# Optimization experiments

Hardware: AMD Instinct MI355X
Metric: run time of the kernel (lower is better)

## Reference

```python
import jax, jax.numpy as jnp
import numpy as np


def setup_inputs() -> dict:
    key = jax.random.key(0)
    k1, k2, k3, k4, k5, k6 = jax.random.split(key, 6)
    Ne, dim_in, dim_out, B, Nr, E = 100000, 128, 128, 4, 8, 200000
    return {
        "H": jax.random.normal(k1, (Ne, dim_in), dtype=jnp.float32),
        "A": jax.random.uniform(k2, (Nr, B), dtype=jnp.float32),
        "V": jax.random.uniform(k3, (B, dim_in, dim_out), dtype=jnp.float32),
        "edge_row": jax.random.randint(k4, (Nr, E), 0, Ne, dtype=jnp.int32),
        "edge_col": jax.random.randint(k5, (Nr, E), 0, Ne, dtype=jnp.int32),
        "edge_val": jax.random.uniform(k6, (Nr, E), dtype=jnp.float32),
    }


def reference(H, A, V, edge_row, edge_col, edge_val):
    # W = einsum('rb,bio->rio', A, V): basis-decomposed relation weights
    Ne = H.shape[0]
    Nr = A.shape[0]
    W = jnp.einsum('rb,bio->rio', A, V)            # [Nr, dim_in, dim_out]
    HxW = jnp.einsum('ni,rio->rno', H, W)          # [Nr, Ne, dim_out]
    # sparse T_r @ HxW_r: gather source rows (cols of T), scale by values,
    # scatter-add into destination rows. Done for all relations at once.
    msgs = HxW[jnp.arange(Nr)[:, None], edge_col] * edge_val[..., None]  # [Nr, E, dim_out]
    out = jax.ops.segment_sum(
        msgs.reshape(-1, msgs.shape[-1]),
        edge_row.reshape(-1),
        num_segments=Ne,
    )  # sum over relations folded into one segment_sum
    return out
```

## Files before the change

### kernel.cpp

```cpp
#include <hip/hip_runtime.h>

typedef __attribute__((ext_vector_type(8))) short short8;
typedef __attribute__((ext_vector_type(4))) float floatx4;

constexpr int DIM   = 128;
constexpr int NB    = 4;
constexpr int NR    = 8;
constexpr int BROWS = 512;
constexpr int BCAP  = 16384;

static __device__ __forceinline__ unsigned short f2bf(float f) {
    unsigned int u = __float_as_uint(f);
    u += 0x7FFFu + ((u >> 16) & 1u);
    return (unsigned short)(u >> 16);
}
static __device__ __forceinline__ float bf_lo(unsigned int h) {
    return __uint_as_float(h << 16);
}
static __device__ __forceinline__ float bf_hi(unsigned int h) {
    return __uint_as_float(h & 0xFFFF0000u);
}

__global__ __launch_bounds__(256) void build_vfrag(
    const float* __restrict__ V, unsigned short* __restrict__ VfragG)
{
    int idx  = blockIdx.x * 256 + threadIdx.x;
    int lane = idx & 63;
    int ks   = (idx >> 6) & 3;
    int ot   = (idx >> 8) & 7;
    int b    = idx >> 11;

    int o  = ot * 16 + (lane & 15);
    int kb = ks * 32 + (lane >> 4) * 8;

    short8 v;
#pragma unroll
    for (int j = 0; j < 8; ++j)
        v[j] = (short)f2bf(V[((size_t)b * DIM + kb + j) * DIM + o]);
    *reinterpret_cast<short8*>(VfragG + (size_t)idx * 8) = v;
}

__global__ __launch_bounds__(256) void build_wfrag(
    const float* __restrict__ A, const float* __restrict__ V,
    unsigned short* __restrict__ Wfrag)
{
    int idx  = blockIdx.x * 256 + threadIdx.x;
    int lane = idx & 63;
    int ks   = (idx >> 6) & 3;
    int ot   = (idx >> 8) & 7;
    int r    = idx >> 11;

    int o     = ot * 16 + (lane & 15);
    int kbase = ks * 32 + (lane >> 4) * 8;

    float a0 = A[r * NB + 0], a1 = A[r * NB + 1];
    float a2 = A[r * NB + 2], a3 = A[r * NB + 3];

    short8 v;
#pragma unroll
    for (int j = 0; j < 8; ++j) {
        int k = kbase + j;
        float w = a0 * V[(0 * DIM + k) * DIM + o]
                + a1 * V[(1 * DIM + k) * DIM + o]
                + a2 * V[(2 * DIM + k) * DIM + o]
                + a3 * V[(3 * DIM + k) * DIM + o];
        v[j] = (short)f2bf(w);
    }
    *reinterpret_cast<short8*>(Wfrag + (size_t)idx * 8) = v;
}

__global__ __launch_bounds__(256) void h_to_bf(
    const float* __restrict__ H, unsigned short* __restrict__ Hbf, int n8)
{
    int i = blockIdx.x * 256 + threadIdx.x;
    if (i >= n8) return;
    const float4* hp = reinterpret_cast<const float4*>(H) + (size_t)i * 2;
    float4 f0 = hp[0];
    float4 f1 = hp[1];
    short8 v;
    v[0] = (short)f2bf(f0.x); v[1] = (short)f2bf(f0.y);
    v[2] = (short)f2bf(f0.z); v[3] = (short)f2bf(f0.w);
    v[4] = (short)f2bf(f1.x); v[5] = (short)f2bf(f1.y);
    v[6] = (short)f2bf(f1.z); v[7] = (short)f2bf(f1.w);
    *reinterpret_cast<short8*>(Hbf + (size_t)i * 8) = v;
}

__global__ __launch_bounds__(256) void bucket_scatter(
    const int* __restrict__ erow, const int* __restrict__ ecol,
    const float* __restrict__ eval, int* __restrict__ bcnt,
    int2* __restrict__ sorted1, int n, int E, int chunk)
{
    __shared__ int cnt[256];
    __shared__ int base[256];
    int t = threadIdx.x;
    cnt[t] = 0;
    __syncthreads();

    int s = blockIdx.x * chunk;
    int e = s + chunk; if (e > n) e = n;

    for (int i = s + t; i < e; i += 256)
        atomicAdd(&cnt[erow[i] >> 9], 1);
    __syncthreads();

    int c = cnt[t];
    base[t] = (c > 0) ? atomicAdd(&bcnt[t], c) : 0;
    cnt[t] = 0;
    __syncthreads();

    for (int i = s + t; i < e; i += 256) {
        int row = erow[i];
        int bkt = row >> 9;
        int rank = atomicAdd(&cnt[bkt], 1);
        int r = (int)((unsigned)i / (unsigned)E);
        int2 m;
        m.x = ((row & (BROWS - 1)) << 20) | (r << 17) | ecol[i];
        m.y = __float_as_int(eval[i]);
        sorted1[(size_t)bkt * BCAP + base[bkt] + rank] = m;
    }
}

__global__ __launch_bounds__(256) void bucket_scan(
    const int* __restrict__ bcnt, int* __restrict__ bstart,
    int* __restrict__ rowStart, int nbuc, int Ne)
{
    __shared__ int sd[256];
    int t = threadIdx.x;
    int c = (t < nbuc) ? bcnt[t] : 0;
    sd[t] = c; __syncthreads();
#pragma unroll
    for (int off = 1; off < 256; off <<= 1) {
        int v = (t >= off) ? sd[t - off] : 0;
        __syncthreads();
        sd[t] += v;
        __syncthreads();
    }
    if (t < nbuc) bstart[t] = sd[t] - c;
    if (t == nbuc - 1) rowStart[Ne] = sd[t];
}

__global__ __launch_bounds__(256) void bucket_sort(
    const int2* __restrict__ sorted1, const int* __restrict__ bcnt,
    const int* __restrict__ bstart, int* __restrict__ rowStart,
    int2* __restrict__ sorted, int Ne)
{
    __shared__ int hcnt[BROWS];
    __shared__ int hoff[BROWS];
    int b = blockIdx.x;
    int t = threadIdx.x;
    hcnt[t] = 0; hcnt[t + 256] = 0;
    __syncthreads();

    int n = bcnt[b];
    const int2* src = sorted1 + (size_t)b * BCAP;

    for (int i = t; i < n; i += 256)
        atomicAdd(&hcnt[(unsigned)src[i].x >> 20], 1);
    __syncthreads();

    if (t == 0) {
        int run = 0;
#pragma unroll 8
        for (int j = 0; j < BROWS; ++j) { hoff[j] = run; run += hcnt[j]; }
    }
    __syncthreads();

    int bs = bstart[b];
    int rs = b * BROWS;
    int nr = Ne - rs; if (nr > BROWS) nr = BROWS;
    for (int j = t; j < nr; j += 256)
        rowStart[rs + j] = bs + hoff[j];

    hcnt[t] = 0; hcnt[t + 256] = 0;
    __syncthreads();

    for (int i = t; i < n; i += 256) {
        int2 m = src[i];
        int lr = (unsigned)m.x >> 20;
        int pos = bs + hoff[lr] + atomicAdd(&hcnt[lr], 1);
        sorted[pos] = m;
    }
}

__global__ __launch_bounds__(256) void agg_kernel(
    const unsigned short* __restrict__ Hbf,
    const int*  __restrict__ rowStart,
    const int2* __restrict__ sorted,
    const float* __restrict__ Aw,
    unsigned short* __restrict__ Agg, int Ne)
{
    int tid  = threadIdx.x;
    int wid  = __builtin_amdgcn_readfirstlane(blockIdx.x * 4 + (tid >> 6));
    if (wid >= Ne) return;
    int lane = tid & 63;

    int s = __builtin_amdgcn_readfirstlane(rowStart[wid]);
    int e = __builtin_amdgcn_readfirstlane(rowStart[wid + 1]);

    const float4* Af = reinterpret_cast<const float4*>(Aw);

    float2 acc[4];
#pragma unroll
    for (int b = 0; b < 4; ++b) { acc[b].x = 0.f; acc[b].y = 0.f; }

    int i = s;
    for (; i + 4 <= e; i += 4) {
        int2 m0 = sorted[i],     m1 = sorted[i + 1];
        int2 m2 = sorted[i + 2], m3 = sorted[i + 3];
        int k0 = __builtin_amdgcn_readfirstlane(m0.x);
        int k1 = __builtin_amdgcn_readfirstlane(m1.x);
        int k2 = __builtin_amdgcn_readfirstlane(m2.x);
        int k3 = __builtin_amdgcn_readfirstlane(m3.x);
        float v0 = __uint_as_float(__builtin_amdgcn_readfirstlane(m0.y));
        float v1 = __uint_as_float(__builtin_amdgcn_readfirstlane(m1.y));
        float v2 = __uint_as_float(__builtin_amdgcn_readfirstlane(m2.y));
        float v3 = __uint_as_float(__builtin_amdgcn_readfirstlane(m3.y));

        unsigned int h0 = reinterpret_cast<const unsigned int*>(
            Hbf + (size_t)(k0 & 0x1FFFF) * DIM)[lane];
        unsigned int h1 = reinterpret_cast<const unsigned int*>(
            Hbf + (size_t)(k1 & 0x1FFFF) * DIM)[lane];
        unsigned int h2 = reinterpret_cast<const unsigned int*>(
            Hbf + (size_t)(k2 & 0x1FFFF) * DIM)[lane];
        unsigned int h3 = reinterpret_cast<const unsigned int*>(
            Hbf + (size_t)(k3 & 0x1FFFF) * DIM)[lane];

        int kk[4] = {k0, k1, k2, k3};
        float vv[4] = {v0, v1, v2, v3};
        unsigned int hh[4] = {h0, h1, h2, h3};
#pragma unroll
        for (int u = 0; u < 4; ++u) {
            float4 a = Af[((unsigned)kk[u] >> 17) & 7];
            float hx = bf_lo(hh[u]), hy = bf_hi(hh[u]);
            float s0 = vv[u] * a.x, s1 = vv[u] * a.y;
            float s2 = vv[u] * a.z, s3 = vv[u] * a.w;
            acc[0].x += s0 * hx; acc[0].y += s0 * hy;
            acc[1].x += s1 * hx; acc[1].y += s1 * hy;
            acc[2].x += s2 * hx; acc[2].y += s2 * hy;
            acc[3].x += s3 * hx; acc[3].y += s3 * hy;
        }
    }
    for (; i < e; ++i) {
        int2 m = sorted[i];
        int k = __builtin_amdgcn_readfirstlane(m.x);
        float v = __uint_as_float(__builtin_amdgcn_readfirstlane(m.y));
        unsigned int h = reinterpret_cast<const unsigned int*>(
            Hbf + (size_t)(k & 0x1FFFF) * DIM)[lane];
        float4 a = Af[((unsigned)k >> 17) & 7];
        float hx = bf_lo(h), hy = bf_hi(h);
        float s0 = v * a.x, s1 = v * a.y, s2 = v * a.z, s3 = v * a.w;
        acc[0].x += s0 * hx; acc[0].y += s0 * hy;
        acc[1].x += s1 * hx; acc[1].y += s1 * hy;
        acc[2].x += s2 * hx; acc[2].y += s2 * hy;
        acc[3].x += s3 * hx; acc[3].y += s3 * hy;
    }

    unsigned short* arow = Agg + (size_t)wid * 512 + lane * 2;
#pragma unroll
    for (int b = 0; b < 4; ++b) {
        unsigned int pk = (unsigned int)f2bf(acc[b].x)
                        | ((unsigned int)f2bf(acc[b].y) << 16);
        *reinterpret_cast<unsigned int*>(arow + b * 128) = pk;
    }
}

__global__ __launch_bounds__(512) void vgemm_kernel(
    const unsigned short* __restrict__ Agg,
    const unsigned short* __restrict__ VfragG,
    float* __restrict__ out, int Ne, int nTiles)
{
    __shared__ short8 ldsV[4096];
    int half = (blockIdx.x >> 3) & 1;
    int blk  = ((blockIdx.x >> 4) << 3) | (blockIdx.x & 7);
    int nblk = gridDim.x >> 1;
    int tid  = threadIdx.x;

    for (int i = tid; i < 4096; i += 512) {
        int lane = i & 63, ks = (i >> 6) & 3, otl = (i >> 8) & 3, b = i >> 10;
        int gi = ((b * 8 + half * 4 + otl) * 4 + ks) * 64 + lane;
        ldsV[i] = reinterpret_cast<const short8*>(VfragG)[gi];
    }
    __syncthreads();

    int wave = tid >> 6;
    int lane = tid & 63;
    int quad = lane >> 4, l15 = lane & 15;

    int wgid = blk * 8 + wave;
    int nw   = nblk * 8;

    for (int tile = wgid; tile < nTiles; tile += nw) {
        int node0 = tile * 16;
        int node  = node0 + l15;
        int rdnode = node < Ne ? node : Ne - 1;

        const short8* bp = reinterpret_cast<const short8*>(Agg)
                         + (size_t)rdnode * 64 + quad;
        short8 bf[16];
#pragma unroll
        for (int b = 0; b < 4; ++b)
#pragma unroll
            for (int ks = 0; ks < 4; ++ks)
                bf[b * 4 + ks] = bp[b * 16 + ks * 4];

        floatx4 acc[4];
#pragma unroll
        for (int o = 0; o < 4; ++o) acc[o] = (floatx4){0.f, 0.f, 0.f, 0.f};

#pragma unroll
        for (int b = 0; b < 4; ++b)
#pragma unroll
            for (int ks = 0; ks < 4; ++ks)
#pragma unroll
                for (int otl = 0; otl < 4; ++otl)
                    acc[otl] = __builtin_amdgcn_mfma_f32_16x16x32_bf16(
                        ldsV[((b * 4 + otl) * 4 + ks) * 64 + lane],
                        bf[b * 4 + ks], acc[otl], 0, 0, 0);

        if (node < Ne) {
            float* orow = out + (size_t)node * DIM + half * 64;
#pragma unroll
            for (int otl = 0; otl < 4; ++otl) {
                float4 st;
                st.x = acc[otl][0]; st.y = acc[otl][1];
                st.z = acc[otl][2]; st.w = acc[otl][3];
                *reinterpret_cast<float4*>(orow + otl * 16 + quad * 4) = st;
            }
        }
    }
}

__global__ __launch_bounds__(256) void rgcn_main(
    const unsigned short* __restrict__ Hbf,
    const unsigned short* __restrict__ Wfrag,
    const int*   __restrict__ erow,
    const int*   __restrict__ ecol,
    const float* __restrict__ eval,
    float*       __restrict__ out,
    int E, int groups_per_rel, int waves_per_rel)
{
    int wid  = blockIdx.x * 4 + (threadIdx.x >> 6);
    int lane = threadIdx.x & 63;
    int r    = wid & 7;
    int wr   = wid >> 3;
    int quad = lane >> 4;
    int l15  = lane & 15;

    short8 b[8][4];
    {
        const short8* wp = reinterpret_cast<const short8*>(
            Wfrag + (size_t)r * 16384);
#pragma unroll
        for (int ot = 0; ot < 8; ++ot)
#pragma unroll
            for (int ks = 0; ks < 4; ++ks)
                b[ot][ks] = wp[(ot * 4 + ks) * 64 + lane];
    }

    for (int g = wr; g < groups_per_rel; g += waves_per_rel) {
        int ebase = r * E + g * 16;
        int   colv = ecol[ebase + l15];
        int   rowv = erow[ebase + l15];
        float valv = eval[ebase + l15];

        short8 a[4];
        const unsigned short* hp = Hbf + (size_t)colv * DIM + quad * 8;
#pragma unroll
        for (int ks = 0; ks < 4; ++ks)
            a[ks] = *reinterpret_cast<const short8*>(hp + ks * 32);

        floatx4 acc[8];
#pragma unroll
        for (int ot = 0; ot < 8; ++ot) acc[ot] = (floatx4){0.f, 0.f, 0.f, 0.f};
#pragma unroll
        for (int ot = 0; ot < 8; ++ot)
#pragma unroll
            for (int ks = 0; ks < 4; ++ks)
                acc[ot] = __builtin_amdgcn_mfma_f32_16x16x32_bf16(
                    a[ks], b[ot][ks], acc[ot], 0, 0, 0);

        int   row4[4];
        float val4[4];
#pragma unroll
        for (int reg = 0; reg < 4; ++reg) {
            int src  = quad * 4 + reg;
            row4[reg] = __shfl(rowv, src, 64);
            val4[reg] = __shfl(valv, src, 64);
        }
#pragma unroll
        for (int ot = 0; ot < 8; ++ot)
#pragma unroll
            for (int reg = 0; reg < 4; ++reg) {
                float m = acc[ot][reg] * val4[reg];
                atomicAdd(out + (size_t)row4[reg] * DIM + ot * 16 + l15, m);
            }
    }
}

extern "C" void kernel_launch(void* const* d_in, const int* in_sizes, int n_in,
                              void* d_out, int out_size, void* d_ws, size_t ws_size,
                              hipStream_t stream)
{
    const float* H    = (const float*)d_in[0];
    const float* A    = (const float*)d_in[1];
    const float* V    = (const float*)d_in[2];
    const int*   erow = (const int*)d_in[3];
    const int*   ecol = (const int*)d_in[4];
    const float* eval = (const float*)d_in[5];
    float* out = (float*)d_out;

    int Ne    = in_sizes[0] / DIM;
    int NEtot = in_sizes[3];
    int E     = NEtot / NR;

    auto al = [](size_t x) { return (x + 255) & ~(size_t)255; };

    int nbuc = (Ne + BROWS - 1) / BROWS;

    size_t offHbf    = 0;
    size_t offVfrag  = offHbf    + al((size_t)Ne * DIM * 2);
    size_t offWfrag  = offVfrag  + al((size_t)8192 * 16);
    size_t offAgg    = offWfrag  + al((size_t)16384 * 16);
    size_t offRow    = offAgg    + al((size_t)Ne * 512 * 2);
    size_t offBcnt   = offRow    + al(((size_t)Ne + 2) * 4);
    size_t offBstart = offBcnt   + al((size_t)256 * 4);
    size_t offSort   = offBstart + al((size_t)256 * 4);
    size_t total     = offSort   + al((size_t)NEtot * 8);

    char* ws = (char*)d_ws;
    unsigned short* Hbf    = (unsigned short*)(ws + offHbf);
    unsigned short* VfragG = (unsigned short*)(ws + offVfrag);
    unsigned short* Wfrag  = (unsigned short*)(ws + offWfrag);

    int n8 = Ne * DIM / 8;
    h_to_bf<<<(n8 + 255) / 256, 256, 0, stream>>>(H, Hbf, n8);

    if (ws_size < total) {
        build_wfrag<<<64, 256, 0, stream>>>(A, V, Wfrag);
        hipMemsetAsync(d_out, 0, (size_t)Ne * DIM * sizeof(float), stream);
        int blocks = 4096;
        int waves_per_rel = blocks * 4 / NR;
        int groups_per_rel = E / 16;
        rgcn_main<<<blocks, 256, 0, stream>>>(Hbf, Wfrag, erow, ecol, eval, out,
                                              E, groups_per_rel, waves_per_rel);
        return;
    }

    unsigned short* Agg      = (unsigned short*)(ws + offAgg);
    int2*           sorted1  = (int2*)(ws + offAgg);
    int*            rowStart = (int*)(ws + offRow);
    int*            bcnt     = (int*)(ws + offBcnt);
    int*            bstart   = (int*)(ws + offBstart);
    int2*           sorted   = (int2*)(ws + offSort);

    build_vfrag<<<32, 256, 0, stream>>>(V, VfragG);

    hipMemsetAsync(bcnt, 0, 256 * 4, stream);
    int sblocks = 512;
    int chunk   = (NEtot + sblocks - 1) / sblocks;
    bucket_scatter<<<sblocks, 256, 0, stream>>>(erow, ecol, eval, bcnt,
                                                sorted1, NEtot, E, chunk);
    bucket_scan<<<1, 256, 0, stream>>>(bcnt, bstart, rowStart, nbuc, Ne);
    bucket_sort<<<nbuc, 256, 0, stream>>>(sorted1, bcnt, bstart, rowStart,
                                          sorted, Ne);

    agg_kernel<<<(Ne + 3) / 4, 256, 0, stream>>>(Hbf, rowStart, sorted, A,
                                                 Agg, Ne);

    int nTiles = (Ne + 15) / 16;
    vgemm_kernel<<<512, 512, 0, stream>>>(Agg, VfragG, out, Ne, nTiles);
}
```

Baseline: 326.6 us.

## Double-buffer Agg loads in transform kernel and unroll edge gather by eight

The per-node aggregation loop now batches eight edges per iteration, issuing all index reads and then all H row loads before the FMAs, which raises memory-level parallelism. The MFMA transform kernel now streams the aggregated B fragments through two four-register ping-pong buffers, prefetching the next basis slice and the next tile's first slice while the current MFMAs run. This is meant to hide global load latency behind compute, at the cost of more live registers and a more complex loop.

```diff
diff --git a/kernel.cpp b/kernel.cpp
--- a/kernel.cpp
+++ b/kernel.cpp
@@ -204,32 +204,22 @@
     for (int b = 0; b < 4; ++b) { acc[b].x = 0.f; acc[b].y = 0.f; }
 
     int i = s;
-    for (; i + 4 <= e; i += 4) {
-        int2 m0 = sorted[i],     m1 = sorted[i + 1];
-        int2 m2 = sorted[i + 2], m3 = sorted[i + 3];
-        int k0 = __builtin_amdgcn_readfirstlane(m0.x);
-        int k1 = __builtin_amdgcn_readfirstlane(m1.x);
-        int k2 = __builtin_amdgcn_readfirstlane(m2.x);
-        int k3 = __builtin_amdgcn_readfirstlane(m3.x);
-        float v0 = __uint_as_float(__builtin_amdgcn_readfirstlane(m0.y));
-        float v1 = __uint_as_float(__builtin_amdgcn_readfirstlane(m1.y));
-        float v2 = __uint_as_float(__builtin_amdgcn_readfirstlane(m2.y));
-        float v3 = __uint_as_float(__builtin_amdgcn_readfirstlane(m3.y));
-
-        unsigned int h0 = reinterpret_cast<const unsigned int*>(
-            Hbf + (size_t)(k0 & 0x1FFFF) * DIM)[lane];
-        unsigned int h1 = reinterpret_cast<const unsigned int*>(
-            Hbf + (size_t)(k1 & 0x1FFFF) * DIM)[lane];
-        unsigned int h2 = reinterpret_cast<const unsigned int*>(
-            Hbf + (size_t)(k2 & 0x1FFFF) * DIM)[lane];
-        unsigned int h3 = reinterpret_cast<const unsigned int*>(
-            Hbf + (size_t)(k3 & 0x1FFFF) * DIM)[lane];
-
-        int kk[4] = {k0, k1, k2, k3};
-        float vv[4] = {v0, v1, v2, v3};
-        unsigned int hh[4] = {h0, h1, h2, h3};
-#pragma unroll
-        for (int u = 0; u < 4; ++u) {
+    for (; i + 8 <= e; i += 8) {
+        int kk[8];
+        float vv[8];
+        unsigned int hh[8];
+#pragma unroll
+        for (int u = 0; u < 8; ++u) {
+            int2 m = sorted[i + u];
+            kk[u] = __builtin_amdgcn_readfirstlane(m.x);
+            vv[u] = __uint_as_float(__builtin_amdgcn_readfirstlane(m.y));
+        }
+#pragma unroll
+        for (int u = 0; u < 8; ++u)
+            hh[u] = reinterpret_cast<const unsigned int*>(
+                Hbf + (size_t)(kk[u] & 0x1FFFF) * DIM)[lane];
+#pragma unroll
+        for (int u = 0; u < 8; ++u) {
             float4 a = Af[((unsigned)kk[u] >> 17) & 7];
             float hx = bf_lo(hh[u]), hy = bf_hi(hh[u]);
             float s0 = vv[u] * a.x, s1 = vv[u] * a.y;
@@ -289,33 +279,75 @@
     int wgid = blk * 8 + wave;
     int nw   = nblk * 8;
 
-    for (int tile = wgid; tile < nTiles; tile += nw) {
-        int node0 = tile * 16;
-        int node  = node0 + l15;
-        int rdnode = node < Ne ? node : Ne - 1;
-
-        const short8* bp = reinterpret_cast<const short8*>(Agg)
-                         + (size_t)rdnode * 64 + quad;
-        short8 bf[16];
-#pragma unroll
-        for (int b = 0; b < 4; ++b)
-#pragma unroll
-            for (int ks = 0; ks < 4; ++ks)
-                bf[b * 4 + ks] = bp[b * 16 + ks * 4];
+    if (wgid >= nTiles) return;
+
+    const short8* AggV = reinterpret_cast<const short8*>(Agg);
+
+    short8 bufA[4], bufB[4];
+
+    const short8* bp;
+    {
+        int node = wgid * 16 + l15;
+        int rd   = node < Ne ? node : Ne - 1;
+        bp = AggV + (size_t)rd * 64 + quad;
+    }
+#pragma unroll
+    for (int ks = 0; ks < 4; ++ks) bufA[ks] = bp[0 * 16 + ks * 4];
+
+    int tile = wgid;
+    for (;;) {
+        int node = tile * 16 + l15;
 
         floatx4 acc[4];
 #pragma unroll
         for (int o = 0; o < 4; ++o) acc[o] = (floatx4){0.f, 0.f, 0.f, 0.f};
 
 #pragma unroll
-        for (int b = 0; b < 4; ++b)
-#pragma unroll
-            for (int ks = 0; ks < 4; ++ks)
-#pragma unroll
-                for (int otl = 0; otl < 4; ++otl)
-                    acc[otl] = __builtin_amdgcn_mfma_f32_16x16x32_bf16(
-                        ldsV[((b * 4 + otl) * 4 + ks) * 64 + lane],
-                        bf[b * 4 + ks], acc[otl], 0, 0, 0);
+        for (int ks = 0; ks < 4; ++ks) bufB[ks] = bp[1 * 16 + ks * 4];
+#pragma unroll
+        for (int ks = 0; ks < 4; ++ks)
+#pragma unroll
+            for (int otl = 0; otl < 4; ++otl)
+                acc[otl] = __builtin_amdgcn_mfma_f32_16x16x32_bf16(
+                    ldsV[((0 * 4 + otl) * 4 + ks) * 64 + lane],
+                    bufA[ks], acc[otl], 0, 0, 0);
+
+#pragma unroll
+        for (int ks = 0; ks < 4; ++ks) bufA[ks] = bp[2 * 16 + ks * 4];
+#pragma unroll
+        for (int ks = 0; ks < 4; ++ks)
+#pragma unroll
+            for (int otl = 0; otl < 4; ++otl)
+                acc[otl] = __builtin_amdgcn_mfma_f32_16x16x32_bf16(
+                    ldsV[((1 * 4 + otl) * 4 + ks) * 64 + lane],
+                    bufB[ks], acc[otl], 0, 0, 0);
+
+#pragma unroll
+        for (int ks = 0; ks < 4; ++ks) bufB[ks] = bp[3 * 16 + ks * 4];
+#pragma unroll
+        for (int ks = 0; ks < 4; ++ks)
+#pragma unroll
+            for (int otl = 0; otl < 4; ++otl)
+                acc[otl] = __builtin_amdgcn_mfma_f32_16x16x32_bf16(
+                    ldsV[((2 * 4 + otl) * 4 + ks) * 64 + lane],
+                    bufA[ks], acc[otl], 0, 0, 0);
+
+        int tn = tile + nw;
+        const short8* bpn = bp;
+        if (tn < nTiles) {
+            int noden = tn * 16 + l15;
+            int rdn   = noden < Ne ? noden : Ne - 1;
+            bpn = AggV + (size_t)rdn * 64 + quad;
+#pragma unroll
+            for (int ks = 0; ks < 4; ++ks) bufA[ks] = bpn[0 * 16 + ks * 4];
+        }
+#pragma unroll
+        for (int ks = 0; ks < 4; ++ks)
+#pragma unroll
+            for (int otl = 0; otl < 4; ++otl)
+                acc[otl] = __builtin_amdgcn_mfma_f32_16x16x32_bf16(
+                    ldsV[((3 * 4 + otl) * 4 + ks) * 64 + lane],
+                    bufB[ks], acc[otl], 0, 0, 0);
 
         if (node < Ne) {
             float* orow = out + (size_t)node * DIM + half * 64;
@@ -327,6 +359,10 @@
                 *reinterpret_cast<float4*>(orow + otl * 16 + quad * 4) = st;
             }
         }
+
+        if (tn >= nTiles) break;
+        tile = tn;
+        bp   = bpn;
     }
 }
 
```

Measured after the change: 358.6 us. 1.1x slower.

## Store aggregated features in MFMA tile-fragment layout and unroll gather by 8

Applied to the files above, without the earlier changes.

The aggregation kernel now writes its bf16 per-basis sums into a tiled layout matching the MFMA B-fragment order, so the GEMM kernel reads each 16-node tile as contiguous short8 vectors instead of strided per-row loads. The gather loop is also unrolled from 4 to 8 edges, with all index loads issued first and then all H row loads, to keep more memory requests in flight. The tiled buffer is padded to a whole number of tiles, and the GEMM no longer clamps out-of-range node reads because the padding rows exist (uninitialized but their results are never stored).

```diff
diff --git a/kernel.cpp b/kernel.cpp
--- a/kernel.cpp
+++ b/kernel.cpp
@@ -187,7 +187,7 @@
     const int*  __restrict__ rowStart,
     const int2* __restrict__ sorted,
     const float* __restrict__ Aw,
-    unsigned short* __restrict__ Agg, int Ne)
+    unsigned short* __restrict__ AggT, int Ne)
 {
     int tid  = threadIdx.x;
     int wid  = __builtin_amdgcn_readfirstlane(blockIdx.x * 4 + (tid >> 6));
@@ -204,32 +204,22 @@
     for (int b = 0; b < 4; ++b) { acc[b].x = 0.f; acc[b].y = 0.f; }
 
     int i = s;
-    for (; i + 4 <= e; i += 4) {
-        int2 m0 = sorted[i],     m1 = sorted[i + 1];
-        int2 m2 = sorted[i + 2], m3 = sorted[i + 3];
-        int k0 = __builtin_amdgcn_readfirstlane(m0.x);
-        int k1 = __builtin_amdgcn_readfirstlane(m1.x);
-        int k2 = __builtin_amdgcn_readfirstlane(m2.x);
-        int k3 = __builtin_amdgcn_readfirstlane(m3.x);
-        float v0 = __uint_as_float(__builtin_amdgcn_readfirstlane(m0.y));
-        float v1 = __uint_as_float(__builtin_amdgcn_readfirstlane(m1.y));
-        float v2 = __uint_as_float(__builtin_amdgcn_readfirstlane(m2.y));
-        float v3 = __uint_as_float(__builtin_amdgcn_readfirstlane(m3.y));
-
-        unsigned int h0 = reinterpret_cast<const unsigned int*>(
-            Hbf + (size_t)(k0 & 0x1FFFF) * DIM)[lane];
-        unsigned int h1 = reinterpret_cast<const unsigned int*>(
-            Hbf + (size_t)(k1 & 0x1FFFF) * DIM)[lane];
-        unsigned int h2 = reinterpret_cast<const unsigned int*>(
-            Hbf + (size_t)(k2 & 0x1FFFF) * DIM)[lane];
-        unsigned int h3 = reinterpret_cast<const unsigned int*>(
-            Hbf + (size_t)(k3 & 0x1FFFF) * DIM)[lane];
-
-        int kk[4] = {k0, k1, k2, k3};
-        float vv[4] = {v0, v1, v2, v3};
-        unsigned int hh[4] = {h0, h1, h2, h3};
-#pragma unroll
-        for (int u = 0; u < 4; ++u) {
+    for (; i + 8 <= e; i += 8) {
+        int kk[8];
+        float vv[8];
+        unsigned int hh[8];
+#pragma unroll
+        for (int u = 0; u < 8; ++u) {
+            int2 m = sorted[i + u];
+            kk[u] = __builtin_amdgcn_readfirstlane(m.x);
+            vv[u] = __uint_as_float(__builtin_amdgcn_readfirstlane(m.y));
+        }
+#pragma unroll
+        for (int u = 0; u < 8; ++u)
+            hh[u] = reinterpret_cast<const unsigned int*>(
+                Hbf + (size_t)(kk[u] & 0x1FFFF) * DIM)[lane];
+#pragma unroll
+        for (int u = 0; u < 8; ++u) {
             float4 a = Af[((unsigned)kk[u] >> 17) & 7];
             float hx = bf_lo(hh[u]), hy = bf_hi(hh[u]);
             float s0 = vv[u] * a.x, s1 = vv[u] * a.y;
@@ -255,17 +245,22 @@
         acc[3].x += s3 * hx; acc[3].y += s3 * hy;
     }
 
-    unsigned short* arow = Agg + (size_t)wid * 512 + lane * 2;
+    int t = wid >> 4, r = wid & 15;
+    size_t base = (size_t)t * 8192 + (size_t)r * 32
+                + (size_t)(lane >> 4) * 512
+                + (size_t)((lane >> 2) & 3) * 8
+                + (size_t)(lane & 3) * 2;
+    unsigned short* arow = AggT + base;
 #pragma unroll
     for (int b = 0; b < 4; ++b) {
         unsigned int pk = (unsigned int)f2bf(acc[b].x)
                         | ((unsigned int)f2bf(acc[b].y) << 16);
-        *reinterpret_cast<unsigned int*>(arow + b * 128) = pk;
+        *reinterpret_cast<unsigned int*>(arow + b * 2048) = pk;
     }
 }
 
 __global__ __launch_bounds__(512) void vgemm_kernel(
-    const unsigned short* __restrict__ Agg,
+    const unsigned short* __restrict__ AggT,
     const unsigned short* __restrict__ VfragG,
     float* __restrict__ out, int Ne, int nTiles)
 {
@@ -289,19 +284,18 @@
     int wgid = blk * 8 + wave;
     int nw   = nblk * 8;
 
+    const short8* AggV = reinterpret_cast<const short8*>(AggT);
+
     for (int tile = wgid; tile < nTiles; tile += nw) {
-        int node0 = tile * 16;
-        int node  = node0 + l15;
-        int rdnode = node < Ne ? node : Ne - 1;
-
-        const short8* bp = reinterpret_cast<const short8*>(Agg)
-                         + (size_t)rdnode * 64 + quad;
+        int node = tile * 16 + l15;
+
+        const short8* bp = AggV + (size_t)tile * 1024 + l15 * 4 + quad;
         short8 bf[16];
 #pragma unroll
         for (int b = 0; b < 4; ++b)
 #pragma unroll
             for (int ks = 0; ks < 4; ++ks)
-                bf[b * 4 + ks] = bp[b * 16 + ks * 4];
+                bf[b * 4 + ks] = bp[b * 256 + ks * 64];
 
         floatx4 acc[4];
 #pragma unroll
@@ -416,12 +410,13 @@
     auto al = [](size_t x) { return (x + 255) & ~(size_t)255; };
 
     int nbuc = (Ne + BROWS - 1) / BROWS;
+    int nTiles = (Ne + 15) / 16;
 
     size_t offHbf    = 0;
     size_t offVfrag  = offHbf    + al((size_t)Ne * DIM * 2);
     size_t offWfrag  = offVfrag  + al((size_t)8192 * 16);
     size_t offAgg    = offWfrag  + al((size_t)16384 * 16);
-    size_t offRow    = offAgg    + al((size_t)Ne * 512 * 2);
+    size_t offRow    = offAgg    + al((size_t)nTiles * 16384);
     size_t offBcnt   = offRow    + al(((size_t)Ne + 2) * 4);
     size_t offBstart = offBcnt   + al((size_t)256 * 4);
     size_t offSort   = offBstart + al((size_t)256 * 4);
@@ -446,7 +441,7 @@
         return;
     }
 
-    unsigned short* Agg      = (unsigned short*)(ws + offAgg);
+    unsigned short* AggT     = (unsigned short*)(ws + offAgg);
     int2*           sorted1  = (int2*)(ws + offAgg);
     int*            rowStart = (int*)(ws + offRow);
     int*            bcnt     = (int*)(ws + offBcnt);
@@ -465,8 +460,7 @@
                                           sorted, Ne);
 
     agg_kernel<<<(Ne + 3) / 4, 256, 0, stream>>>(Hbf, rowStart, sorted, A,
-                                                 Agg, Ne);
-
-    int nTiles = (Ne + 15) / 16;
-    vgemm_kernel<<<512, 512, 0, stream>>>(Agg, VfragG, out, Ne, nTiles);
-}
+                                                 AggT, Ne);
+
+    vgemm_kernel<<<512, 512, 0, stream>>>(AggT, VfragG, out, Ne, nTiles);
+}
```

Result: no change. 327.9 us (+0.4%).
